# Performance work log

Hardware: AMD Instinct MI355X
Metric: run time of the kernel (lower is better)

## Reference

```python
import jax, jax.numpy as jnp
import numpy as np

NL, D, ED, N, K, DT_RANK, V, L, B = 24, 768, 1536, 16, 4, 48, 1024, 512, 2


def setup_inputs() -> dict:
    key = jax.random.key(0)
    ks = jax.random.split(key, 12)
    s = 0.02
    rn = lambda k, shape: jax.random.normal(k, shape, dtype=jnp.float32) * s
    return {
        "src": jax.random.randint(ks[0], (L, B), 0, V),
        "embed": rn(ks[1], (V, D)),
        "norm_w": jnp.ones((NL, D), jnp.float32),
        "in_proj": rn(ks[2], (NL, 2 * ED, D)),
        "conv_w": rn(ks[3], (NL, ED, K)) * 10.0,  # ~N(0, 0.2)
        "conv_b": jnp.zeros((NL, ED), jnp.float32),
        "x_proj": rn(ks[4], (NL, DT_RANK + 2 * N, ED)),
        "dt_w": rn(ks[5], (NL, ED, DT_RANK)),
        # softplus(dt_b) in ~[0.007, 0.05], like HF Mamba's dt init range
        "dt_b": jax.random.uniform(ks[6], (NL, ED), minval=-5.0, maxval=-3.0),
        # S4D-real init: A = -[1..N]
        "A_log": jnp.log(jnp.broadcast_to(jnp.arange(1, N + 1, dtype=jnp.float32), (NL, ED, N))),
        "Dp": jnp.ones((NL, ED), jnp.float32),
        "out_proj": rn(ks[7], (NL, D, ED)),
        "normf_w": jnp.ones((D,), jnp.float32),
    }


def _rmsnorm(x, w, eps=1e-5):
    return x * jax.lax.rsqrt(jnp.mean(x * x, axis=-1, keepdims=True) + eps) * w


def _forward(src, embed, norm_w, in_proj, conv_w, conv_b, x_proj, dt_w, dt_b,
             A_log, Dp, out_proj, normf_w):
    ids = src.T  # [B, L] (module does src.T.contiguous())
    h = embed[ids]  # [B, L, D]

    def layer(x, p):
        nw, W_in, cw, cb, W_x, W_dt, b_dt, a_log, d, W_out = p
        ug = jnp.einsum('bld,ed->ble', _rmsnorm(x, nw), W_in)  # [B,L,2ED]
        u, g = jnp.split(ug, 2, axis=-1)
        # depthwise causal conv1d, kernel K
        up = jnp.pad(u, ((0, 0), (K - 1, 0), (0, 0)))
        uc = sum(up[:, k:k + u.shape[1], :] * cw[:, k] for k in range(K)) + cb
        uc = jax.nn.silu(uc)
        # SSM parameters
        sp = jnp.einsum('ble,se->bls', uc, W_x)
        dt_r, Bm, Cm = jnp.split(sp, [DT_RANK, DT_RANK + N], axis=-1)
        dt = jax.nn.softplus(jnp.einsum('blr,er->ble', dt_r, W_dt) + b_dt)  # [B,L,ED]
        A = -jnp.exp(a_log)  # [ED, N]

        def step(hst, ins):
            dt_t, B_t, C_t, u_t = ins  # [B,ED],[B,N],[B,N],[B,ED]
            dA = jnp.exp(dt_t[..., None] * A)            # [B,ED,N]
            hst = dA * hst + (dt_t * u_t)[..., None] * B_t[:, None, :]
            y = jnp.einsum('ben,bn->be', hst, C_t)
            return hst, y

        h0 = jnp.zeros((x.shape[0], ED, N), x.dtype)
        xs = (dt.transpose(1, 0, 2), Bm.transpose(1, 0, 2),
              Cm.transpose(1, 0, 2), uc.transpose(1, 0, 2))
        _, ys = jax.lax.scan(step, h0, xs)                # [L,B,ED]
        y = ys.transpose(1, 0, 2) + uc * d
        y = y * jax.nn.silu(g)
        return x + jnp.einsum('ble,de->bld', y, W_out), None

    h, _ = jax.lax.scan(layer, h, (norm_w, in_proj, conv_w, conv_b, x_proj,
                                   dt_w, dt_b, A_log, Dp, out_proj))
    h = _rmsnorm(h, normf_w)
    logits = jnp.einsum('bld,vd->blv', h, embed)  # tied lm_head, no bias
    return logits.transpose(1, 0, 2)  # [L, B, V] (module returns x.transpose(0,1))


def reference(src, embed, norm_w, in_proj, conv_w, conv_b, x_proj, dt_w, dt_b,
              A_log, Dp, out_proj, normf_w):
    return _forward(src, embed, norm_w, in_proj, conv_w, conv_b, x_proj, dt_w,
                    dt_b, A_log, Dp, out_proj, normf_w)
```

## Files before the change

### kernel.cpp

```cpp
#include <hip/hip_runtime.h>
#include <hip/hip_bf16.h>
#include <math.h>

#define NL   24
#define DDIM 768
#define ED   1536
#define NST  16
#define KC   4
#define DTR  48
#define VV   1024
#define LL   512
#define BB   2
#define MM   (BB*LL)
#define SP   80

#define NC   32
#define CL   (LL/NC)

#define XKS  16
#define XKC  (ED/XKS)

#define OPS  4
#define OPK  (ED/OPS)

typedef unsigned short u16;
typedef __bf16 bf16x8 __attribute__((ext_vector_type(8)));
typedef float  floatx4 __attribute__((ext_vector_type(4)));
typedef unsigned short ushort4v __attribute__((ext_vector_type(4)));

typedef const __attribute__((address_space(1))) void gvoid_t;
typedef __attribute__((address_space(3))) void svoid_t;

#define GLD16(g, l) __builtin_amdgcn_global_load_lds((gvoid_t*)(g), (svoid_t*)(l), 16, 0, 0)

__device__ __forceinline__ float softplusf(float x) {
    return fmaxf(x, 0.0f) + log1pf(expf(-fabsf(x)));
}
__device__ __forceinline__ float siluf(float x) {
    return x / (1.0f + expf(-x));
}
__device__ __forceinline__ u16 f2bf(float x) {
    unsigned int u = __builtin_bit_cast(unsigned int, x);
    u += 0x7FFFu + ((u >> 16) & 1u);
    return (u16)(u >> 16);
}

__global__ __launch_bounds__(256) void cvt_bf16_kernel(
        const float* __restrict__ in, u16* __restrict__ out, int n4)
{
    int stride = gridDim.x * 256;
    for (int i = blockIdx.x * 256 + threadIdx.x; i < n4; i += stride) {
        float4 v = reinterpret_cast<const float4*>(in)[i];
        ushort4v o = {f2bf(v.x), f2bf(v.y), f2bf(v.z), f2bf(v.w)};
        reinterpret_cast<ushort4v*>(out)[i] = o;
    }
}

__global__ __launch_bounds__(256) void embed_kernel(
        const int* __restrict__ src, const float* __restrict__ emb,
        float* __restrict__ h)
{
    int m = blockIdx.x;
    int b = m >> 9;
    int l = m & (LL - 1);
    int v = src[l * BB + b];
    const float* er = emb + (size_t)v * DDIM;
    float* hr = h + (size_t)m * DDIM;
    for (int d = threadIdx.x; d < DDIM; d += 256) hr[d] = er[d];
}

__global__ __launch_bounds__(256) void rmsnorm_res_kernel(
        float* __restrict__ h, const float* __restrict__ part, int nz,
        const float* __restrict__ w, u16* __restrict__ o)
{
    __shared__ float red[4];
    int m = blockIdx.x, tid = threadIdx.x;
    float* hr = h + (size_t)m * DDIM;
    float v0 = hr[tid], v1 = hr[tid + 256], v2 = hr[tid + 512];
    for (int z = 0; z < nz; z++) {
        const float* pr = part + ((size_t)z * MM + m) * DDIM;
        v0 += pr[tid]; v1 += pr[tid + 256]; v2 += pr[tid + 512];
    }
    if (nz > 0) {
        hr[tid] = v0; hr[tid + 256] = v1; hr[tid + 512] = v2;
    }
    float s = v0 * v0 + v1 * v1 + v2 * v2;
    #pragma unroll
    for (int off = 32; off; off >>= 1) s += __shfl_down(s, off);
    if ((tid & 63) == 0) red[tid >> 6] = s;
    __syncthreads();
    float tot = red[0] + red[1] + red[2] + red[3];
    float scale = rsqrtf(tot * (1.0f / DDIM) + 1e-5f);
    u16* orow = o + (size_t)m * DDIM;
    orow[tid]       = f2bf(v0 * scale * w[tid]);
    orow[tid + 256] = f2bf(v1 * scale * w[tid + 256]);
    orow[tid + 512] = f2bf(v2 * scale * w[tid + 512]);
}

template<int MODE>
__global__ __launch_bounds__(256) void gemm_bf16_d(
        const u16* __restrict__ A, int lda,
        const u16* __restrict__ W, int ldb,
        float* __restrict__ C, int ldc,
        int Kper)
{
    __shared__ __attribute__((aligned(16))) u16 As[2][128 * 64];
    __shared__ __attribute__((aligned(16))) u16 Bs[2][64 * 64];
    int tid  = threadIdx.x;
    int lane = tid & 63;
    int wave = tid >> 6;
    int wm = wave >> 1, wn = wave & 1;
    int colBase = blockIdx.x * 64;
    int rowBase = blockIdx.y * 128;
    int k0 = blockIdx.z * Kper;

    floatx4 acc[4][2];
    #pragma unroll
    for (int i = 0; i < 4; i++)
        #pragma unroll
        for (int j = 0; j < 2; j++)
            acc[i][j] = (floatx4){0.f, 0.f, 0.f, 0.f};

    int kc = lane >> 4;
    int lm = lane & 15;

    const u16* Ap[4];
    #pragma unroll
    for (int j = 0; j < 4; j++) {
        int q = (wave * 4 + j) * 64 + lane;
        int r = q >> 3, cg = (q & 7) ^ (r & 7);
        Ap[j] = A + (size_t)(rowBase + r) * lda + k0 + cg * 8;
    }
    const u16* Wp[2];
    #pragma unroll
    for (int j = 0; j < 2; j++) {
        int q = (wave * 2 + j) * 64 + lane;
        int r = q >> 3, cg = (q & 7) ^ (r & 7);
        Wp[j] = W + (size_t)(colBase + r) * ldb + k0 + cg * 8;
    }

    auto stage = [&](int buf, int kk) {
        u16* as = &As[buf][0];
        u16* bs = &Bs[buf][0];
        #pragma unroll
        for (int j = 0; j < 4; j++) GLD16(Ap[j] + kk, as + (wave * 4 + j) * 512);
        #pragma unroll
        for (int j = 0; j < 2; j++) GLD16(Wp[j] + kk, bs + (wave * 2 + j) * 512);
    };

    int nt = Kper >> 6;
    stage(0, 0);
    __syncthreads();
    for (int t = 0; t < nt; t++) {
        int cur = t & 1;
        if (t + 1 < nt) stage(cur ^ 1, (t + 1) * 64);
        #pragma unroll
        for (int ks = 0; ks < 2; ks++) {
            int ck = ks * 4 + kc;
            bf16x8 af[4], bw[2];
            #pragma unroll
            for (int i = 0; i < 4; i++) {
                int m = wm * 64 + i * 16 + lm;
                af[i] = *reinterpret_cast<const bf16x8*>(
                    &As[cur][m * 64 + ((ck ^ (m & 7)) * 8)]);
            }
            #pragma unroll
            for (int j = 0; j < 2; j++) {
                int n = wn * 32 + j * 16 + lm;
                bw[j] = *reinterpret_cast<const bf16x8*>(
                    &Bs[cur][n * 64 + ((ck ^ (n & 7)) * 8)]);
            }
            #pragma unroll
            for (int i = 0; i < 4; i++)
                #pragma unroll
                for (int j = 0; j < 2; j++)
                    acc[i][j] = __builtin_amdgcn_mfma_f32_16x16x32_bf16(
                        af[i], bw[j], acc[i][j], 0, 0, 0);
        }
        __syncthreads();
    }

    float* Cz = (MODE == 4) ? (C + (size_t)blockIdx.z * MM * ldc) : C;
    int c4 = (lane >> 4) * 4;
    #pragma unroll
    for (int i = 0; i < 4; i++) {
        #pragma unroll
        for (int j = 0; j < 2; j++) {
            floatx4 v = acc[i][j];
            int col = colBase + wn * 32 + j * 16 + lm;
            #pragma unroll
            for (int p = 0; p < 4; p++) {
                int row = rowBase + wm * 64 + i * 16 + c4 + p;
                if (MODE == 3) {
                    int l = row & (LL - 1), b = row >> 9;
                    Cz[((size_t)l * BB + b) * ldc + col] = v[p];
                } else {
                    Cz[(size_t)row * ldc + col] = v[p];
                }
            }
        }
    }
}

__global__ __launch_bounds__(256) void sgemm_nt(
        const float* __restrict__ A, int lda,
        const float* __restrict__ W, int ldb,
        float* __restrict__ C, int ldc,
        int Nmat, int Kdim, int mode, const float* __restrict__ bias)
{
    __shared__ float As[16][65];
    __shared__ float Ws[16][65];
    int tid = threadIdx.x;
    int tx = tid & 15, ty = tid >> 4;
    int rowBase = blockIdx.x * 64;
    int colBase = blockIdx.y * 64;
    float acc[4][4] = {};

    for (int kk = 0; kk < Kdim; kk += 16) {
        #pragma unroll
        for (int i = 0; i < 4; i++) {
            int idx = tid + i * 256;
            int r = idx >> 4, kc = idx & 15;
            As[kc][r] = A[(size_t)(rowBase + r) * lda + kk + kc];
            int cG = colBase + r;
            Ws[kc][r] = (cG < Nmat) ? W[(size_t)cG * ldb + kk + kc] : 0.0f;
        }
        __syncthreads();
        #pragma unroll
        for (int k = 0; k < 16; k++) {
            float av[4], bv[4];
            #pragma unroll
            for (int i = 0; i < 4; i++) av[i] = As[k][ty + 16 * i];
            #pragma unroll
            for (int j = 0; j < 4; j++) bv[j] = Ws[k][tx + 16 * j];
            #pragma unroll
            for (int i = 0; i < 4; i++)
                #pragma unroll
                for (int j = 0; j < 4; j++)
                    acc[i][j] = fmaf(av[i], bv[j], acc[i][j]);
        }
        __syncthreads();
    }

    #pragma unroll
    for (int i = 0; i < 4; i++) {
        int m = rowBase + ty + 16 * i;
        #pragma unroll
        for (int j = 0; j < 4; j++) {
            int n = colBase + tx + 16 * j;
            if (n >= Nmat) continue;
            float v = acc[i][j];
            if (mode == 0) {
                C[(size_t)m * ldc + n] = v;
            } else {
                C[(size_t)m * ldc + n] = softplusf(v + bias[n]);
            }
        }
    }
}

__global__ __launch_bounds__(256) void xproj_conv_partial(
        const float* __restrict__ ug, const float* __restrict__ cw,
        const float* __restrict__ cb, const float* __restrict__ W,
        float* __restrict__ part, float* __restrict__ ucb)
{
    __shared__ float As[16][65];
    __shared__ float Ws[16][88];
    int tid = threadIdx.x;
    int tx = tid & 15;
    int ty = tid >> 4;
    int rowBase = blockIdx.x * 64;
    int k0 = blockIdx.y * XKC;
    float acc[4][5] = {};

    for (int kk = 0; kk < XKC; kk += 16) {
        #pragma unroll
        for (int i = 0; i < 4; i++) {
            int idx = tid + i * 256;
            int r = idx >> 4, kc = idx & 15;
            int m = rowBase + r;
            int e = k0 + kk + kc;
            int b = m >> 9, l = m & (LL - 1);
            float a = cb[e];
            #pragma unroll
            for (int k = 0; k < KC; k++) {
                int ll = l + k - (KC - 1);
                float uv = (ll >= 0) ? ug[((size_t)(b * LL + ll)) * (2 * ED) + e] : 0.0f;
                a = fmaf(uv, cw[e * KC + k], a);
            }
            a = siluf(a);
            As[kc][r] = a;
            ucb[(size_t)m * ED + e] = a;
        }
        #pragma unroll
        for (int i = 0; i < 5; i++) {
            int idx = tid + i * 256;
            int c = idx >> 4, kc = idx & 15;
            Ws[kc][c] = W[(size_t)c * ED + k0 + kk + kc];
        }
        __syncthreads();
        #pragma unroll
        for (int k = 0; k < 16; k++) {
            float av[4], bv[5];
            #pragma unroll
            for (int i = 0; i < 4; i++) av[i] = As[k][ty + 16 * i];
            #pragma unroll
            for (int j = 0; j < 5; j++) bv[j] = Ws[k][tx + 16 * j];
            #pragma unroll
            for (int i = 0; i < 4; i++)
                #pragma unroll
                for (int j = 0; j < 5; j++)
                    acc[i][j] = fmaf(av[i], bv[j], acc[i][j]);
        }
        __syncthreads();
    }

    float* p = part + ((size_t)blockIdx.y * MM + rowBase) * SP;
    #pragma unroll
    for (int i = 0; i < 4; i++)
        #pragma unroll
        for (int j = 0; j < 5; j++)
            p[(ty + 16 * i) * SP + tx + 16 * j] = acc[i][j];
}

__global__ __launch_bounds__(256) void xproj_reduce(
        const float* __restrict__ part, float* __restrict__ spb)
{
    int idx = blockIdx.x * 256 + threadIdx.x;
    float4 s = {0.f, 0.f, 0.f, 0.f};
    #pragma unroll
    for (int ks = 0; ks < XKS; ks++) {
        float4 v = reinterpret_cast<const float4*>(part + (size_t)ks * MM * SP)[idx];
        s.x += v.x; s.y += v.y; s.z += v.z; s.w += v.w;
    }
    reinterpret_cast<float4*>(spb)[idx] = s;
}

__global__ __launch_bounds__(256) void scan_pass1(
        const float* __restrict__ dtb, const float* __restrict__ ucb,
        const float* __restrict__ spb, const float* __restrict__ A_log,
        float* __restrict__ hfin, float* __restrict__ sumdt)
{
    int e = blockIdx.x * 256 + threadIdx.x;
    int c = blockIdx.y;
    int b = blockIdx.z;
    float a[NST], h[NST];
    const float4* ap = reinterpret_cast<const float4*>(A_log + (size_t)e * NST);
    #pragma unroll
    for (int q = 0; q < 4; q++) {
        float4 v = ap[q];
        a[4*q+0] = -expf(v.x); a[4*q+1] = -expf(v.y);
        a[4*q+2] = -expf(v.z); a[4*q+3] = -expf(v.w);
    }
    #pragma unroll
    for (int n = 0; n < NST; n++) h[n] = 0.0f;
    float sdt = 0.0f;
    int m0 = b * LL + c * CL;
    for (int l = 0; l < CL; l++) {
        int m = m0 + l;
        float dtv = dtb[(size_t)m * ED + e];
        float ucv = ucb[(size_t)m * ED + e];
        const float4* bp = reinterpret_cast<const float4*>(spb + (size_t)m * SP + DTR);
        float x = dtv * ucv;
        sdt += dtv;
        #pragma unroll
        for (int q = 0; q < 4; q++) {
            float4 bv = bp[q];
            h[4*q+0] = fmaf(expf(dtv * a[4*q+0]), h[4*q+0], x * bv.x);
            h[4*q+1] = fmaf(expf(dtv * a[4*q+1]), h[4*q+1], x * bv.y);
            h[4*q+2] = fmaf(expf(dtv * a[4*q+2]), h[4*q+2], x * bv.z);
            h[4*q+3] = fmaf(expf(dtv * a[4*q+3]), h[4*q+3], x * bv.w);
        }
    }
    float* hf = hfin + (((size_t)(b * ED + e)) * NC + c) * NST;
    #pragma unroll
    for (int n = 0; n < NST; n++) hf[n] = h[n];
    sumdt[((size_t)(b * ED + e)) * NC + c] = sdt;
}

__global__ __launch_bounds__(256) void scan_mid(
        const float* __restrict__ hfin, const float* __restrict__ sumdt,
        const float* __restrict__ A_log, float* __restrict__ hstart)
{
    int gid = blockIdx.x * 256 + threadIdx.x;
    int n = gid & 15;
    int be = gid >> 4;
    int e = be % ED;
    float a = -expf(A_log[(size_t)e * NST + n]);
    float h = 0.0f;
    const float* hf = hfin + (size_t)be * NC * NST;
    const float* sd = sumdt + (size_t)be * NC;
    float* hs = hstart + (size_t)be * NC * NST;
    for (int c = 0; c < NC; c++) {
        hs[c * NST + n] = h;
        h = fmaf(expf(a * sd[c]), h, hf[c * NST + n]);
    }
}

__global__ __launch_bounds__(256) void scan_pass2(
        const float* __restrict__ dtb, const float* __restrict__ ucb,
        const float* __restrict__ spb, const float* __restrict__ ugb,
        const float* __restrict__ A_log, const float* __restrict__ Dp,
        const float* __restrict__ hstart, u16* __restrict__ yb)
{
    int e = blockIdx.x * 256 + threadIdx.x;
    int c = blockIdx.y;
    int b = blockIdx.z;
    float a[NST], h[NST];
    const float4* ap = reinterpret_cast<const float4*>(A_log + (size_t)e * NST);
    #pragma unroll
    for (int q = 0; q < 4; q++) {
        float4 v = ap[q];
        a[4*q+0] = -expf(v.x); a[4*q+1] = -expf(v.y);
        a[4*q+2] = -expf(v.z); a[4*q+3] = -expf(v.w);
    }
    const float* hs = hstart + (((size_t)(b * ED + e)) * NC + c) * NST;
    #pragma unroll
    for (int n = 0; n < NST; n++) h[n] = hs[n];
    float dpv = Dp[e];
    int m0 = b * LL + c * CL;
    for (int l = 0; l < CL; l++) {
        int m = m0 + l;
        float dtv = dtb[(size_t)m * ED + e];
        float ucv = ucb[(size_t)m * ED + e];
        const float4* bp = reinterpret_cast<const float4*>(spb + (size_t)m * SP + DTR);
        const float4* cp = reinterpret_cast<const float4*>(spb + (size_t)m * SP + DTR + NST);
        float g = ugb[(size_t)m * (2 * ED) + ED + e];
        float x = dtv * ucv;
        float y0 = 0.0f, y1 = 0.0f, y2 = 0.0f, y3 = 0.0f;
        #pragma unroll
        for (int q = 0; q < 4; q++) {
            float4 bv = bp[q];
            float4 cv = cp[q];
            h[4*q+0] = fmaf(expf(dtv * a[4*q+0]), h[4*q+0], x * bv.x);
            h[4*q+1] = fmaf(expf(dtv * a[4*q+1]), h[4*q+1], x * bv.y);
            h[4*q+2] = fmaf(expf(dtv * a[4*q+2]), h[4*q+2], x * bv.z);
            h[4*q+3] = fmaf(expf(dtv * a[4*q+3]), h[4*q+3], x * bv.w);
            y0 = fmaf(h[4*q+0], cv.x, y0);
            y1 = fmaf(h[4*q+1], cv.y, y1);
            y2 = fmaf(h[4*q+2], cv.z, y2);
            y3 = fmaf(h[4*q+3], cv.w, y3);
        }
        float yv = (y0 + y1) + (y2 + y3) + ucv * dpv;
        yb[(size_t)m * ED + e] = f2bf(yv * siluf(g));
    }
}

extern "C" void kernel_launch(void* const* d_in, const int* in_sizes, int n_in,
                              void* d_out, int out_size, void* d_ws, size_t ws_size,
                              hipStream_t stream) {
    const int*   src    = (const int*)  d_in[0];
    const float* emb    = (const float*)d_in[1];
    const float* norm_w = (const float*)d_in[2];
    const float* in_prj = (const float*)d_in[3];
    const float* conv_w = (const float*)d_in[4];
    const float* conv_b = (const float*)d_in[5];
    const float* x_prj  = (const float*)d_in[6];
    const float* dt_w   = (const float*)d_in[7];
    const float* dt_b   = (const float*)d_in[8];
    const float* A_log  = (const float*)d_in[9];
    const float* Dp     = (const float*)d_in[10];
    const float* out_p  = (const float*)d_in[11];
    const float* normf  = (const float*)d_in[12];
    float* out = (float*)d_out;

    float* ws    = (float*)d_ws;
    float* h     = ws;
    float* xn_f  = h     + (size_t)MM * DDIM;
    float* ug    = xn_f  + (size_t)MM * DDIM;
    float* ucb   = ug    + (size_t)MM * 2 * ED;
    float* spb   = ucb   + (size_t)MM * ED;
    float* dtbf  = spb   + (size_t)MM * SP;
    float* yb_f  = dtbf  + (size_t)MM * ED;
    float* hfin  = yb_f  + (size_t)MM * ED;
    float* sumdt = hfin  + (size_t)BB * ED * NC * NST;
    float* hstart= sumdt + (size_t)BB * ED * NC;
    float* wend  = hstart+ (size_t)BB * ED * NC * NST;
    float* xpart = hfin;

    u16* xn = (u16*)xn_f;
    u16* yb = (u16*)yb_f;
    u16* wbf_in  = (u16*)wend;
    u16* wbf_out = wbf_in  + (size_t)NL * 2 * ED * DDIM;
    u16* wbf_emb = wbf_out + (size_t)NL * DDIM * ED;
    float* opart = (float*)(wbf_emb + (size_t)VV * DDIM);

    cvt_bf16_kernel<<<2048, 256, 0, stream>>>(in_prj, wbf_in, NL * 2 * ED * DDIM / 4);
    cvt_bf16_kernel<<<2048, 256, 0, stream>>>(out_p, wbf_out, NL * DDIM * ED / 4);
    cvt_bf16_kernel<<<256, 256, 0, stream>>>(emb, wbf_emb, VV * DDIM / 4);

    embed_kernel<<<MM, 256, 0, stream>>>(src, emb, h);

    for (int layer = 0; layer < NL; layer++) {
        rmsnorm_res_kernel<<<MM, 256, 0, stream>>>(
            h, opart, layer == 0 ? 0 : OPS, norm_w + (size_t)layer * DDIM, xn);
        gemm_bf16_d<0><<<dim3(2 * ED / 64, MM / 128, 1), 256, 0, stream>>>(
            xn, DDIM, wbf_in + (size_t)layer * 2 * ED * DDIM, DDIM,
            ug, 2 * ED, DDIM);
        xproj_conv_partial<<<dim3(MM / 64, XKS), 256, 0, stream>>>(
            ug, conv_w + (size_t)layer * ED * KC, conv_b + (size_t)layer * ED,
            x_prj + (size_t)layer * SP * ED, xpart, ucb);
        xproj_reduce<<<MM * SP / 1024, 256, 0, stream>>>(xpart, spb);
        sgemm_nt<<<dim3(MM / 64, ED / 64), 256, 0, stream>>>(
            spb, SP, dt_w + (size_t)layer * ED * DTR, DTR,
            dtbf, ED, ED, DTR, 1, dt_b + (size_t)layer * ED);
        scan_pass1<<<dim3(ED / 256, NC, BB), 256, 0, stream>>>(
            dtbf, ucb, spb, A_log + (size_t)layer * ED * NST, hfin, sumdt);
        scan_mid<<<BB * ED * NST / 256, 256, 0, stream>>>(
            hfin, sumdt, A_log + (size_t)layer * ED * NST, hstart);
        scan_pass2<<<dim3(ED / 256, NC, BB), 256, 0, stream>>>(
            dtbf, ucb, spb, ug, A_log + (size_t)layer * ED * NST,
            Dp + (size_t)layer * ED, hstart, yb);
        gemm_bf16_d<4><<<dim3(DDIM / 64, MM / 128, OPS), 256, 0, stream>>>(
            yb, ED, wbf_out + (size_t)layer * DDIM * ED, ED,
            opart, DDIM, OPK);
    }

    rmsnorm_res_kernel<<<MM, 256, 0, stream>>>(h, opart, OPS, normf, xn);
    gemm_bf16_d<3><<<dim3(VV / 64, MM / 128, 1), 256, 0, stream>>>(
        xn, DDIM, wbf_emb, DDIM, out, VV, DDIM);
}
```

Before: 3.531 ms.

## Fuse dt projection into scan passes and fold chunk-prefix combine into pass2

Removes the separate fp32 dt GEMM+softplus kernel and instead computes dt per timestep inside both scan passes from shared-memory staged x_proj output and per-thread dt weights in registers. The scan_mid kernel is removed; each pass2 block recomputes its starting state by serially combining previous chunk summaries. The bf16 GEMM gains a templated N-tile width so the final lm_head uses narrower tiles for more blocks. This trades duplicated dt arithmetic (done twice) and redundant prefix work for fewer launches and no dt buffer round-trip.

```diff
diff --git a/kernel.cpp b/kernel.cpp
--- a/kernel.cpp
+++ b/kernel.cpp
@@ -97,7 +97,7 @@
     orow[tid + 512] = f2bf(v2 * scale * w[tid + 512]);
 }
 
-template<int MODE>
+template<int BNF, int MODE>
 __global__ __launch_bounds__(256) void gemm_bf16_d(
         const u16* __restrict__ A, int lda,
         const u16* __restrict__ W, int ldb,
@@ -105,20 +105,20 @@
         int Kper)
 {
     __shared__ __attribute__((aligned(16))) u16 As[2][128 * 64];
-    __shared__ __attribute__((aligned(16))) u16 Bs[2][64 * 64];
+    __shared__ __attribute__((aligned(16))) u16 Bs[2][BNF * 32 * 64];
     int tid  = threadIdx.x;
     int lane = tid & 63;
     int wave = tid >> 6;
     int wm = wave >> 1, wn = wave & 1;
-    int colBase = blockIdx.x * 64;
+    int colBase = blockIdx.x * (BNF * 32);
     int rowBase = blockIdx.y * 128;
     int k0 = blockIdx.z * Kper;
 
-    floatx4 acc[4][2];
+    floatx4 acc[4][BNF];
     #pragma unroll
     for (int i = 0; i < 4; i++)
         #pragma unroll
-        for (int j = 0; j < 2; j++)
+        for (int j = 0; j < BNF; j++)
             acc[i][j] = (floatx4){0.f, 0.f, 0.f, 0.f};
 
     int kc = lane >> 4;
@@ -131,10 +131,10 @@
         int r = q >> 3, cg = (q & 7) ^ (r & 7);
         Ap[j] = A + (size_t)(rowBase + r) * lda + k0 + cg * 8;
     }
-    const u16* Wp[2];
-    #pragma unroll
-    for (int j = 0; j < 2; j++) {
-        int q = (wave * 2 + j) * 64 + lane;
+    const u16* Wp[BNF];
+    #pragma unroll
+    for (int j = 0; j < BNF; j++) {
+        int q = (wave * BNF + j) * 64 + lane;
         int r = q >> 3, cg = (q & 7) ^ (r & 7);
         Wp[j] = W + (size_t)(colBase + r) * ldb + k0 + cg * 8;
     }
@@ -145,7 +145,7 @@
         #pragma unroll
         for (int j = 0; j < 4; j++) GLD16(Ap[j] + kk, as + (wave * 4 + j) * 512);
         #pragma unroll
-        for (int j = 0; j < 2; j++) GLD16(Wp[j] + kk, bs + (wave * 2 + j) * 512);
+        for (int j = 0; j < BNF; j++) GLD16(Wp[j] + kk, bs + (wave * BNF + j) * 512);
     };
 
     int nt = Kper >> 6;
@@ -157,7 +157,7 @@
         #pragma unroll
         for (int ks = 0; ks < 2; ks++) {
             int ck = ks * 4 + kc;
-            bf16x8 af[4], bw[2];
+            bf16x8 af[4], bw[BNF];
             #pragma unroll
             for (int i = 0; i < 4; i++) {
                 int m = wm * 64 + i * 16 + lm;
@@ -165,15 +165,15 @@
                     &As[cur][m * 64 + ((ck ^ (m & 7)) * 8)]);
             }
             #pragma unroll
-            for (int j = 0; j < 2; j++) {
-                int n = wn * 32 + j * 16 + lm;
+            for (int j = 0; j < BNF; j++) {
+                int n = wn * (BNF * 16) + j * 16 + lm;
                 bw[j] = *reinterpret_cast<const bf16x8*>(
                     &Bs[cur][n * 64 + ((ck ^ (n & 7)) * 8)]);
             }
             #pragma unroll
             for (int i = 0; i < 4; i++)
                 #pragma unroll
-                for (int j = 0; j < 2; j++)
+                for (int j = 0; j < BNF; j++)
                     acc[i][j] = __builtin_amdgcn_mfma_f32_16x16x32_bf16(
                         af[i], bw[j], acc[i][j], 0, 0, 0);
         }
@@ -185,9 +185,9 @@
     #pragma unroll
     for (int i = 0; i < 4; i++) {
         #pragma unroll
-        for (int j = 0; j < 2; j++) {
+        for (int j = 0; j < BNF; j++) {
             floatx4 v = acc[i][j];
-            int col = colBase + wn * 32 + j * 16 + lm;
+            int col = colBase + wn * (BNF * 16) + j * 16 + lm;
             #pragma unroll
             for (int p = 0; p < 4; p++) {
                 int row = rowBase + wm * 64 + i * 16 + c4 + p;
@@ -202,63 +202,6 @@
     }
 }
 
-__global__ __launch_bounds__(256) void sgemm_nt(
-        const float* __restrict__ A, int lda,
-        const float* __restrict__ W, int ldb,
-        float* __restrict__ C, int ldc,
-        int Nmat, int Kdim, int mode, const float* __restrict__ bias)
-{
-    __shared__ float As[16][65];
-    __shared__ float Ws[16][65];
-    int tid = threadIdx.x;
-    int tx = tid & 15, ty = tid >> 4;
-    int rowBase = blockIdx.x * 64;
-    int colBase = blockIdx.y * 64;
-    float acc[4][4] = {};
-
-    for (int kk = 0; kk < Kdim; kk += 16) {
-        #pragma unroll
-        for (int i = 0; i < 4; i++) {
-            int idx = tid + i * 256;
-            int r = idx >> 4, kc = idx & 15;
-            As[kc][r] = A[(size_t)(rowBase + r) * lda + kk + kc];
-            int cG = colBase + r;
-            Ws[kc][r] = (cG < Nmat) ? W[(size_t)cG * ldb + kk + kc] : 0.0f;
-        }
-        __syncthreads();
-        #pragma unroll
-        for (int k = 0; k < 16; k++) {
-            float av[4], bv[4];
-            #pragma unroll
-            for (int i = 0; i < 4; i++) av[i] = As[k][ty + 16 * i];
-            #pragma unroll
-            for (int j = 0; j < 4; j++) bv[j] = Ws[k][tx + 16 * j];
-            #pragma unroll
-            for (int i = 0; i < 4; i++)
-                #pragma unroll
-                for (int j = 0; j < 4; j++)
-                    acc[i][j] = fmaf(av[i], bv[j], acc[i][j]);
-        }
-        __syncthreads();
-    }
-
-    #pragma unroll
-    for (int i = 0; i < 4; i++) {
-        int m = rowBase + ty + 16 * i;
-        #pragma unroll
-        for (int j = 0; j < 4; j++) {
-            int n = colBase + tx + 16 * j;
-            if (n >= Nmat) continue;
-            float v = acc[i][j];
-            if (mode == 0) {
-                C[(size_t)m * ldc + n] = v;
-            } else {
-                C[(size_t)m * ldc + n] = softplusf(v + bias[n]);
-            }
-        }
-    }
-}
-
 __global__ __launch_bounds__(256) void xproj_conv_partial(
         const float* __restrict__ ug, const float* __restrict__ cw,
         const float* __restrict__ cb, const float* __restrict__ W,
@@ -337,13 +280,29 @@
 }
 
 __global__ __launch_bounds__(256) void scan_pass1(
-        const float* __restrict__ dtb, const float* __restrict__ ucb,
-        const float* __restrict__ spb, const float* __restrict__ A_log,
+        const float* __restrict__ spb, const float* __restrict__ dt_w,
+        const float* __restrict__ dt_b, const float* __restrict__ ucb,
+        const float* __restrict__ A_log,
         float* __restrict__ hfin, float* __restrict__ sumdt)
 {
-    int e = blockIdx.x * 256 + threadIdx.x;
+    __shared__ float sp_s[CL][SP];
+    int tid = threadIdx.x;
+    int e = blockIdx.x * 256 + tid;
     int c = blockIdx.y;
     int b = blockIdx.z;
+    int m0 = b * LL + c * CL;
+    for (int i = tid; i < CL * SP / 4; i += 256) {
+        reinterpret_cast<float4*>(&sp_s[0][0])[i] =
+            reinterpret_cast<const float4*>(spb + (size_t)m0 * SP)[i];
+    }
+    float wdt[DTR];
+    const float4* wp = reinterpret_cast<const float4*>(dt_w + (size_t)e * DTR);
+    #pragma unroll
+    for (int q = 0; q < DTR / 4; q++) {
+        float4 v = wp[q];
+        wdt[4*q+0] = v.x; wdt[4*q+1] = v.y; wdt[4*q+2] = v.z; wdt[4*q+3] = v.w;
+    }
+    float bias = dt_b[e];
     float a[NST], h[NST];
     const float4* ap = reinterpret_cast<const float4*>(A_log + (size_t)e * NST);
     #pragma unroll
@@ -354,18 +313,26 @@
     }
     #pragma unroll
     for (int n = 0; n < NST; n++) h[n] = 0.0f;
+    __syncthreads();
+
     float sdt = 0.0f;
-    int m0 = b * LL + c * CL;
     for (int l = 0; l < CL; l++) {
-        int m = m0 + l;
-        float dtv = dtb[(size_t)m * ED + e];
-        float ucv = ucb[(size_t)m * ED + e];
-        const float4* bp = reinterpret_cast<const float4*>(spb + (size_t)m * SP + DTR);
+        float dacc = 0.0f;
+        #pragma unroll
+        for (int q = 0; q < DTR / 4; q++) {
+            float4 s4 = *reinterpret_cast<const float4*>(&sp_s[l][4 * q]);
+            dacc = fmaf(s4.x, wdt[4*q+0], dacc);
+            dacc = fmaf(s4.y, wdt[4*q+1], dacc);
+            dacc = fmaf(s4.z, wdt[4*q+2], dacc);
+            dacc = fmaf(s4.w, wdt[4*q+3], dacc);
+        }
+        float dtv = softplusf(dacc + bias);
+        float ucv = ucb[(size_t)(m0 + l) * ED + e];
         float x = dtv * ucv;
         sdt += dtv;
         #pragma unroll
         for (int q = 0; q < 4; q++) {
-            float4 bv = bp[q];
+            float4 bv = *reinterpret_cast<const float4*>(&sp_s[l][DTR + 4 * q]);
             h[4*q+0] = fmaf(expf(dtv * a[4*q+0]), h[4*q+0], x * bv.x);
             h[4*q+1] = fmaf(expf(dtv * a[4*q+1]), h[4*q+1], x * bv.y);
             h[4*q+2] = fmaf(expf(dtv * a[4*q+2]), h[4*q+2], x * bv.z);
@@ -378,34 +345,31 @@
     sumdt[((size_t)(b * ED + e)) * NC + c] = sdt;
 }
 
-__global__ __launch_bounds__(256) void scan_mid(
-        const float* __restrict__ hfin, const float* __restrict__ sumdt,
-        const float* __restrict__ A_log, float* __restrict__ hstart)
-{
-    int gid = blockIdx.x * 256 + threadIdx.x;
-    int n = gid & 15;
-    int be = gid >> 4;
-    int e = be % ED;
-    float a = -expf(A_log[(size_t)e * NST + n]);
-    float h = 0.0f;
-    const float* hf = hfin + (size_t)be * NC * NST;
-    const float* sd = sumdt + (size_t)be * NC;
-    float* hs = hstart + (size_t)be * NC * NST;
-    for (int c = 0; c < NC; c++) {
-        hs[c * NST + n] = h;
-        h = fmaf(expf(a * sd[c]), h, hf[c * NST + n]);
-    }
-}
-
 __global__ __launch_bounds__(256) void scan_pass2(
-        const float* __restrict__ dtb, const float* __restrict__ ucb,
-        const float* __restrict__ spb, const float* __restrict__ ugb,
-        const float* __restrict__ A_log, const float* __restrict__ Dp,
-        const float* __restrict__ hstart, u16* __restrict__ yb)
-{
-    int e = blockIdx.x * 256 + threadIdx.x;
+        const float* __restrict__ spb, const float* __restrict__ dt_w,
+        const float* __restrict__ dt_b, const float* __restrict__ ucb,
+        const float* __restrict__ ugb, const float* __restrict__ A_log,
+        const float* __restrict__ Dp, const float* __restrict__ hfin,
+        const float* __restrict__ sumdt, u16* __restrict__ yb)
+{
+    __shared__ float sp_s[CL][SP];
+    int tid = threadIdx.x;
+    int e = blockIdx.x * 256 + tid;
     int c = blockIdx.y;
     int b = blockIdx.z;
+    int m0 = b * LL + c * CL;
+    for (int i = tid; i < CL * SP / 4; i += 256) {
+        reinterpret_cast<float4*>(&sp_s[0][0])[i] =
+            reinterpret_cast<const float4*>(spb + (size_t)m0 * SP)[i];
+    }
+    float wdt[DTR];
+    const float4* wp = reinterpret_cast<const float4*>(dt_w + (size_t)e * DTR);
+    #pragma unroll
+    for (int q = 0; q < DTR / 4; q++) {
+        float4 v = wp[q];
+        wdt[4*q+0] = v.x; wdt[4*q+1] = v.y; wdt[4*q+2] = v.z; wdt[4*q+3] = v.w;
+    }
+    float bias = dt_b[e];
     float a[NST], h[NST];
     const float4* ap = reinterpret_cast<const float4*>(A_log + (size_t)e * NST);
     #pragma unroll
@@ -414,24 +378,48 @@
         a[4*q+0] = -expf(v.x); a[4*q+1] = -expf(v.y);
         a[4*q+2] = -expf(v.z); a[4*q+3] = -expf(v.w);
     }
-    const float* hs = hstart + (((size_t)(b * ED + e)) * NC + c) * NST;
-    #pragma unroll
-    for (int n = 0; n < NST; n++) h[n] = hs[n];
+    #pragma unroll
+    for (int n = 0; n < NST; n++) h[n] = 0.0f;
+    {
+        size_t be = (size_t)(b * ED + e);
+        const float* sd = sumdt + be * NC;
+        const float* hfp = hfin + be * NC * NST;
+        for (int cp = 0; cp < c; cp++) {
+            float f = sd[cp];
+            const float4* hq = reinterpret_cast<const float4*>(hfp + cp * NST);
+            #pragma unroll
+            for (int q = 0; q < 4; q++) {
+                float4 hv = hq[q];
+                h[4*q+0] = fmaf(expf(a[4*q+0] * f), h[4*q+0], hv.x);
+                h[4*q+1] = fmaf(expf(a[4*q+1] * f), h[4*q+1], hv.y);
+                h[4*q+2] = fmaf(expf(a[4*q+2] * f), h[4*q+2], hv.z);
+                h[4*q+3] = fmaf(expf(a[4*q+3] * f), h[4*q+3], hv.w);
+            }
+        }
+    }
     float dpv = Dp[e];
-    int m0 = b * LL + c * CL;
+    __syncthreads();
+
     for (int l = 0; l < CL; l++) {
         int m = m0 + l;
-        float dtv = dtb[(size_t)m * ED + e];
+        float dacc = 0.0f;
+        #pragma unroll
+        for (int q = 0; q < DTR / 4; q++) {
+            float4 s4 = *reinterpret_cast<const float4*>(&sp_s[l][4 * q]);
+            dacc = fmaf(s4.x, wdt[4*q+0], dacc);
+            dacc = fmaf(s4.y, wdt[4*q+1], dacc);
+            dacc = fmaf(s4.z, wdt[4*q+2], dacc);
+            dacc = fmaf(s4.w, wdt[4*q+3], dacc);
+        }
+        float dtv = softplusf(dacc + bias);
         float ucv = ucb[(size_t)m * ED + e];
-        const float4* bp = reinterpret_cast<const float4*>(spb + (size_t)m * SP + DTR);
-        const float4* cp = reinterpret_cast<const float4*>(spb + (size_t)m * SP + DTR + NST);
         float g = ugb[(size_t)m * (2 * ED) + ED + e];
         float x = dtv * ucv;
         float y0 = 0.0f, y1 = 0.0f, y2 = 0.0f, y3 = 0.0f;
         #pragma unroll
         for (int q = 0; q < 4; q++) {
-            float4 bv = bp[q];
-            float4 cv = cp[q];
+            float4 bv = *reinterpret_cast<const float4*>(&sp_s[l][DTR + 4 * q]);
+            float4 cv = *reinterpret_cast<const float4*>(&sp_s[l][DTR + NST + 4 * q]);
             h[4*q+0] = fmaf(expf(dtv * a[4*q+0]), h[4*q+0], x * bv.x);
             h[4*q+1] = fmaf(expf(dtv * a[4*q+1]), h[4*q+1], x * bv.y);
             h[4*q+2] = fmaf(expf(dtv * a[4*q+2]), h[4*q+2], x * bv.z);
@@ -470,12 +458,10 @@
     float* ug    = xn_f  + (size_t)MM * DDIM;
     float* ucb   = ug    + (size_t)MM * 2 * ED;
     float* spb   = ucb   + (size_t)MM * ED;
-    float* dtbf  = spb   + (size_t)MM * SP;
-    float* yb_f  = dtbf  + (size_t)MM * ED;
+    float* yb_f  = spb   + (size_t)MM * SP;
     float* hfin  = yb_f  + (size_t)MM * ED;
     float* sumdt = hfin  + (size_t)BB * ED * NC * NST;
-    float* hstart= sumdt + (size_t)BB * ED * NC;
-    float* wend  = hstart+ (size_t)BB * ED * NC * NST;
+    float* wend  = sumdt + (size_t)BB * ED * NC;
     float* xpart = hfin;
 
     u16* xn = (u16*)xn_f;
@@ -494,29 +480,26 @@
     for (int layer = 0; layer < NL; layer++) {
         rmsnorm_res_kernel<<<MM, 256, 0, stream>>>(
             h, opart, layer == 0 ? 0 : OPS, norm_w + (size_t)layer * DDIM, xn);
-        gemm_bf16_d<0><<<dim3(2 * ED / 64, MM / 128, 1), 256, 0, stream>>>(
+        gemm_bf16_d<2, 0><<<dim3(2 * ED / 64, MM / 128, 1), 256, 0, stream>>>(
             xn, DDIM, wbf_in + (size_t)layer * 2 * ED * DDIM, DDIM,
             ug, 2 * ED, DDIM);
         xproj_conv_partial<<<dim3(MM / 64, XKS), 256, 0, stream>>>(
             ug, conv_w + (size_t)layer * ED * KC, conv_b + (size_t)layer * ED,
             x_prj + (size_t)layer * SP * ED, xpart, ucb);
         xproj_reduce<<<MM * SP / 1024, 256, 0, stream>>>(xpart, spb);
-        sgemm_nt<<<dim3(MM / 64, ED / 64), 256, 0, stream>>>(
-            spb, SP, dt_w + (size_t)layer * ED * DTR, DTR,
-            dtbf, ED, ED, DTR, 1, dt_b + (size_t)layer * ED);
         scan_pass1<<<dim3(ED / 256, NC, BB), 256, 0, stream>>>(
-            dtbf, ucb, spb, A_log + (size_t)layer * ED * NST, hfin, sumdt);
-        scan_mid<<<BB * ED * NST / 256, 256, 0, stream>>>(
-            hfin, sumdt, A_log + (size_t)layer * ED * NST, hstart);
+            spb, dt_w + (size_t)layer * ED * DTR, dt_b + (size_t)layer * ED,
+            ucb, A_log + (size_t)layer * ED * NST, hfin, sumdt);
         scan_pass2<<<dim3(ED / 256, NC, BB), 256, 0, stream>>>(
-            dtbf, ucb, spb, ug, A_log + (size_t)layer * ED * NST,
-            Dp + (size_t)layer * ED, hstart, yb);
-        gemm_bf16_d<4><<<dim3(DDIM / 64, MM / 128, OPS), 256, 0, stream>>>(
+            spb, dt_w + (size_t)layer * ED * DTR, dt_b + (size_t)layer * ED,
+            ucb, ug, A_log + (size_t)layer * ED * NST,
+            Dp + (size_t)layer * ED, hfin, sumdt, yb);
+        gemm_bf16_d<2, 4><<<dim3(DDIM / 64, MM / 128, OPS), 256, 0, stream>>>(
             yb, ED, wbf_out + (size_t)layer * DDIM * ED, ED,
             opart, DDIM, OPK);
     }
 
     rmsnorm_res_kernel<<<MM, 256, 0, stream>>>(h, opart, OPS, normf, xn);
-    gemm_bf16_d<3><<<dim3(VV / 64, MM / 128, 1), 256, 0, stream>>>(
+    gemm_bf16_d<1, 3><<<dim3(VV / 32, MM / 128, 1), 256, 0, stream>>>(
         xn, DDIM, wbf_emb, DDIM, out, VV, DDIM);
 }
```

New measurement: 4.191 ms. +18.7%, slower.
